# Optimization experiments

Measured on AMD Instinct MI355X. Metric: run time of the kernel, lower is better.

## Reference

```python
import jax, jax.numpy as jnp
from jax import lax
import numpy as np

B, T, IN = 32, 1024, 64
H1, H2, OUT = 512, 256, 1


def setup_inputs() -> dict:
    key = jax.random.key(0)
    ks = jax.random.split(key, 13)
    s = 0.05
    return {
        "x": jax.random.normal(ks[0], (B, T, IN), jnp.float32),
        # PyTorch LSTMCell params, gate order i,f,g,o stacked along first dim (4H)
        "W_ih0": jax.random.normal(ks[1], (4 * H1, IN), jnp.float32) * s,
        "W_hh0": jax.random.normal(ks[2], (4 * H1, H1), jnp.float32) * s,
        "b_ih0": jax.random.normal(ks[3], (4 * H1,), jnp.float32) * s,
        "b_hh0": jax.random.normal(ks[4], (4 * H1,), jnp.float32) * s,
        "W_ih1": jax.random.normal(ks[5], (4 * H1, H1), jnp.float32) * s,
        "W_hh1": jax.random.normal(ks[6], (4 * H1, H1), jnp.float32) * s,
        "b_ih1": jax.random.normal(ks[7], (4 * H1,), jnp.float32) * s,
        "b_hh1": jax.random.normal(ks[8], (4 * H1,), jnp.float32) * s,
        "W1": jax.random.normal(ks[9], (H2, H1), jnp.float32) * s,
        "b1": jax.random.normal(ks[10], (H2,), jnp.float32) * s,
        "W2": jax.random.normal(ks[11], (OUT, H2), jnp.float32) * s,
        "b2": jax.random.normal(ks[12], (OUT,), jnp.float32) * s,
    }


def _lstm_layer(x, W_ih, W_hh, b_ih, b_hh):
    """Unrolled LSTM layer. x: (B,T,F) -> hidden, cell sequences (B,T,H)."""
    b, t, _ = x.shape
    h = W_hh.shape[1]
    # precompute input contribution to gates for all timesteps: (B,T,4H)
    xg = jnp.einsum('btf,gf->btg', x, W_ih) + b_ih + b_hh

    def step(carry, xg_t):
        hx, cx = carry
        gates = xg_t + hx @ W_hh.T  # (B,4H)
        i, f, g, o = jnp.split(gates, 4, axis=-1)
        cx = jax.nn.sigmoid(f) * cx + jax.nn.sigmoid(i) * jnp.tanh(g)
        hx = jax.nn.sigmoid(o) * jnp.tanh(cx)
        return (hx, cx), (hx, cx)

    h0 = jnp.zeros((b, h), x.dtype)
    _, (hs, cs) = lax.scan(step, (h0, h0), jnp.swapaxes(xg, 0, 1))
    return jnp.swapaxes(hs, 0, 1), jnp.swapaxes(cs, 0, 1)


def reference(x, W_ih0, W_hh0, b_ih0, b_hh0, W_ih1, W_hh1, b_ih1, b_hh1,
              W1, b1, W2, b2):
    h0s, c0s = _lstm_layer(x, W_ih0, W_hh0, b_ih0, b_hh0)
    h1s, c1s = _lstm_layer(h0s, W_ih1, W_hh1, b_ih1, b_hh1)
    # MLP head (dropout layers are identity in eval mode)
    hidden = jax.nn.relu(h1s @ W1.T + b1)
    out = hidden @ W2.T + b2  # (B,T,OUT)
    return out, ((h0s, h1s), (c0s, c1s))
```

## Files before the change

kernel.cpp:

```cpp
#include <hip/hip_runtime.h>

#define HSEQ 16777216
#define NPL 32
#define NBLK 64

typedef __attribute__((ext_vector_type(8))) __bf16 bf16x8;
typedef __attribute__((ext_vector_type(4))) float f32x4;
typedef unsigned long long u64;

__global__ __launch_bounds__(256) void prep_x(const float* __restrict__ x,
                                              __bf16* __restrict__ xbf) {
    int idx = blockIdx.x * 256 + threadIdx.x;
    int k4 = idx & 15;
    int t  = (idx >> 4) & 1023;
    int m  = idx >> 14;
    float4 v = ((const float4*)x)[idx];
    __bf16* d = xbf + (size_t)t * 2048 + m * 64 + k4 * 4;
    d[0] = (__bf16)v.x; d[1] = (__bf16)v.y; d[2] = (__bf16)v.z; d[3] = (__bf16)v.w;
}

__device__ inline float sigf(float v) { return 1.f / (1.f + expf(-v)); }

__device__ __forceinline__ u64 llc_load(const u64* p) {
    return __hip_atomic_load(p, __ATOMIC_RELAXED, __HIP_MEMORY_SCOPE_AGENT);
}
__device__ __forceinline__ void llc_store(u64* p, u64 v) {
    __hip_atomic_store(p, v, __ATOMIC_RELAXED, __HIP_MEMORY_SCOPE_AGENT);
}

__device__ __forceinline__ void stfrag(char* smem, int kt_base, int m, int kc4, u64 v) {
    int k0   = kc4 << 2;
    int kt   = kt_base + (k0 >> 5);
    int sub  = (k0 >> 3) & 3;
    int half = (k0 >> 2) & 1;
    int slot = ((kt << 1) + (m >> 4)) * 64 + (sub << 4) + (m & 15);
    int byte = ((slot << 4) ^ (((slot >> 7) & 7) << 4)) + (half << 3);
    *(u64*)(smem + byte) = v;
}

template<int LAYER>
__device__ __forceinline__ void run_layer(
    int sub, int tid, int blk,
    const __bf16* __restrict__ xbf,
    const float* __restrict__ Wih, const float* __restrict__ Whh,
    const float* __restrict__ bih, const float* __restrict__ bhh,
    const __bf16* __restrict__ hin_buf,
    __bf16* __restrict__ hself_buf,
    int* flags,
    float* __restrict__ hs_out, float* __restrict__ cs_out,
    char* smem)
{
    constexpr int KT = LAYER ? 32 : 18;
    const int hd0   = sub * 16;
    const int lane  = tid & 63;
    const int wid   = tid >> 6;
    const int mtile = wid & 1;
    const int ntile = wid >> 1;
    const int koff  = (lane >> 4) << 3;

    bf16x8 wfr[KT];
    {
        const int n   = lane & 15;
        const int row = ntile * 512 + hd0 + n;
#pragma unroll
        for (int kt = 0; kt < KT; ++kt) {
            int k0 = kt * 32 + koff;
            const float* wp;
            if (LAYER == 0)
                wp = (k0 < 64) ? (Wih + (size_t)row * 64 + k0)
                               : (Whh + (size_t)row * 512 + (k0 - 64));
            else
                wp = (k0 < 512) ? (Wih + (size_t)row * 512 + k0)
                                : (Whh + (size_t)row * 512 + (k0 - 512));
            float4 f0 = ((const float4*)wp)[0];
            float4 f1 = ((const float4*)wp)[1];
            bf16x8 w;
            w[0]=(__bf16)f0.x; w[1]=(__bf16)f0.y; w[2]=(__bf16)f0.z; w[3]=(__bf16)f0.w;
            w[4]=(__bf16)f1.x; w[5]=(__bf16)f1.y; w[6]=(__bf16)f1.z; w[7]=(__bf16)f1.w;
            wfr[kt] = w;
        }
    }
    const int um = tid >> 4, uq = tid & 15;
    const float bi0 = bih[hd0 + uq]        + bhh[hd0 + uq];
    const float bi1 = bih[512 + hd0 + uq]  + bhh[512 + hd0 + uq];
    const float bi2 = bih[1024 + hd0 + uq] + bhh[1024 + hd0 + uq];
    const float bi3 = bih[1536 + hd0 + uq] + bhh[1536 + hd0 + uq];
    float creg = 0.f;

    float*  gates  = (float*)smem;
    __bf16* hstage = (__bf16*)(smem + 8448);

    for (int s = 0; s < 1025; ++s) {
        const bool active = LAYER ? (s >= 1) : (s < 1024);
        const int t = LAYER ? (s - 1) : s;

        if (s > 0 && tid < NBLK) {
            int* fp = flags + tid * 16;
            while (__hip_atomic_load(fp, __ATOMIC_RELAXED, __HIP_MEMORY_SCOPE_AGENT) < s)
                __builtin_amdgcn_s_sleep(1);
        }
        __syncthreads();

        if (active) {
            if (LAYER == 0) {
                u64 vx = *(const u64*)(xbf + (size_t)t * 2048 + (tid >> 4) * 64 + (tid & 15) * 4);
                const u64* hs = (const u64*)(hself_buf + ((s & 1) ^ 1) * (32 * 512));
                u64 v[8];
#pragma unroll
                for (int i = 0; i < 8; ++i) v[i] = llc_load(hs + tid + i * 512);
                stfrag(smem, 0, tid >> 4, tid & 15, vx);
#pragma unroll
                for (int i = 0; i < 8; ++i) {
                    int c = tid + i * 512;
                    stfrag(smem, 2, c >> 7, c & 127, v[i]);
                }
            } else {
                const u64* h0 = (const u64*)(hin_buf + ((s & 1) ^ 1) * (32 * 512));
                const u64* h1 = (const u64*)(hself_buf + ((s & 1) ^ 1) * (32 * 512));
                u64 v0[8], v1[8];
#pragma unroll
                for (int i = 0; i < 8; ++i) v0[i] = llc_load(h0 + tid + i * 512);
#pragma unroll
                for (int i = 0; i < 8; ++i) v1[i] = llc_load(h1 + tid + i * 512);
#pragma unroll
                for (int i = 0; i < 8; ++i) {
                    int c = tid + i * 512;
                    stfrag(smem, 0, c >> 7, c & 127, v0[i]);
                }
#pragma unroll
                for (int i = 0; i < 8; ++i) {
                    int c = tid + i * 512;
                    stfrag(smem, 16, c >> 7, c & 127, v1[i]);
                }
            }
        }
        __syncthreads();

        f32x4 acc0 = {0.f,0.f,0.f,0.f}, acc1 = {0.f,0.f,0.f,0.f};
        if (active) {
            const int sb = (mtile * 64 + lane) << 4;
#pragma unroll
            for (int kt = 0; kt < KT; ++kt) {
                bf16x8 a = *(const bf16x8*)(smem + ((sb ^ ((kt & 7) << 4)) + kt * 2048));
                if (kt & 1) acc1 = __builtin_amdgcn_mfma_f32_16x16x32_bf16(a, wfr[kt], acc1, 0, 0, 0);
                else        acc0 = __builtin_amdgcn_mfma_f32_16x16x32_bf16(a, wfr[kt], acc0, 0, 0, 0);
            }
        }
        __syncthreads();

        if (active) {
            f32x4 acc = acc0 + acc1;
#pragma unroll
            for (int r = 0; r < 4; ++r)
                gates[(mtile * 16 + ((lane >> 4) << 2) + r) * 65 + ntile * 16 + (lane & 15)] = acc[r];
        }
        __syncthreads();

        if (active) {
            float gi = gates[um * 65 + uq]      + bi0;
            float gf = gates[um * 65 + 16 + uq] + bi1;
            float gg = gates[um * 65 + 32 + uq] + bi2;
            float go = gates[um * 65 + 48 + uq] + bi3;
            float si = sigf(gi), sf = sigf(gf), so = sigf(go);
            creg = sf * creg + si * tanhf(gg);
            float hval = so * tanhf(creg);
            hstage[um * 16 + uq] = (__bf16)hval;
            __builtin_nontemporal_store(hval, &hs_out[((size_t)um * 1024 + t) * 512 + hd0 + uq]);
            __builtin_nontemporal_store(creg, &cs_out[((size_t)um * 1024 + t) * 512 + hd0 + uq]);
        }
        __syncthreads();

        if (active && tid < 128) {
            int m = tid >> 2, q4 = tid & 3;
            u64 v = *(const u64*)(hstage + m * 16 + q4 * 4);
            u64* hout = (u64*)(hself_buf + (s & 1) * (32 * 512));
            llc_store(hout + m * 128 + (hd0 >> 2) + q4, v);
        }
        __syncthreads();

        if (s < 1024 && tid == 0)
            __hip_atomic_store(flags + blk * 16, s + 1, __ATOMIC_RELAXED, __HIP_MEMORY_SCOPE_AGENT);
    }
}

__global__ __launch_bounds__(512, 1) void lstm2(
    const __bf16* __restrict__ xbf,
    const float* __restrict__ Wih0, const float* __restrict__ Whh0,
    const float* __restrict__ bih0, const float* __restrict__ bhh0,
    const float* __restrict__ Wih1, const float* __restrict__ Whh1,
    const float* __restrict__ bih1, const float* __restrict__ bhh1,
    __bf16* __restrict__ h0buf, __bf16* __restrict__ h1buf,
    int* flags, float* __restrict__ dout)
{
    __shared__ alignas(16) char smem[65536];
    const int tid = threadIdx.x, blk = blockIdx.x;
    float* hsbase = dout + 32768;
    if (blk < NPL)
        run_layer<0>(blk, tid, blk, xbf, Wih0, Whh0, bih0, bhh0, nullptr, h0buf,
                     flags, hsbase, hsbase + 2 * (size_t)HSEQ, smem);
    else
        run_layer<1>(blk - NPL, tid, blk, xbf, Wih1, Whh1, bih1, bhh1, h0buf, h1buf,
                     flags, hsbase + (size_t)HSEQ, hsbase + 3 * (size_t)HSEQ, smem);
}

__global__ __launch_bounds__(256) void head_kernel(
    const float* __restrict__ h1s, const float* __restrict__ W1,
    const float* __restrict__ b1,  const float* __restrict__ W2,
    const float* __restrict__ b2,  float* __restrict__ out)
{
    __shared__ alignas(16) float hl[16][512];
    __shared__ float red[16][257];
    const int tid = threadIdx.x;
    const size_t tok0 = (size_t)blockIdx.x * 16;

    const float4* src = (const float4*)(h1s + tok0 * 512);
    float4* dst = (float4*)(&hl[0][0]);
    for (int i = tid; i < 2048; i += 256) dst[i] = src[i];
    __syncthreads();

    float acc[16];
#pragma unroll
    for (int i = 0; i < 16; ++i) acc[i] = 0.f;
    const float4* wrow = (const float4*)(W1 + (size_t)tid * 512);
    for (int k4 = 0; k4 < 128; ++k4) {
        float4 w = wrow[k4];
#pragma unroll
        for (int i = 0; i < 16; ++i) {
            float4 h = ((const float4*)&hl[i][0])[k4];
            acc[i] += w.x * h.x + w.y * h.y + w.z * h.z + w.w * h.w;
        }
    }
    float w2 = W2[tid];
    float bb1 = b1[tid];
#pragma unroll
    for (int i = 0; i < 16; ++i) {
        float hid = acc[i] + bb1;
        red[i][tid] = w2 * (hid > 0.f ? hid : 0.f);
    }
    __syncthreads();
    if (tid < 16) {
        float ssum = b2[0];
        for (int j = 0; j < 256; ++j) ssum += red[tid][j];
        out[tok0 + tid] = ssum;
    }
}

extern "C" void kernel_launch(void* const* d_in, const int* in_sizes, int n_in,
                              void* d_out, int out_size, void* d_ws, size_t ws_size,
                              hipStream_t stream) {
    const float* x    = (const float*)d_in[0];
    const float* Wih0 = (const float*)d_in[1];
    const float* Whh0 = (const float*)d_in[2];
    const float* bih0 = (const float*)d_in[3];
    const float* bhh0 = (const float*)d_in[4];
    const float* Wih1 = (const float*)d_in[5];
    const float* Whh1 = (const float*)d_in[6];
    const float* bih1 = (const float*)d_in[7];
    const float* bhh1 = (const float*)d_in[8];
    const float* W1   = (const float*)d_in[9];
    const float* b1   = (const float*)d_in[10];
    const float* W2   = (const float*)d_in[11];
    const float* b2   = (const float*)d_in[12];
    float* out = (float*)d_out;

    char* ws = (char*)d_ws;
    int*    flags = (int*)ws;
    __bf16* h0buf = (__bf16*)(ws + 4096);
    __bf16* h1buf = (__bf16*)(ws + 4096 + 65536);
    __bf16* xbf   = (__bf16*)(ws + 4096 + 131072);

    hipMemsetAsync(ws, 0, 4096 + 131072, stream);

    prep_x<<<2048, 256, 0, stream>>>(x, xbf);

    const __bf16* xbf_c = xbf;
    void* args[] = {
        (void*)&xbf_c,
        (void*)&Wih0, (void*)&Whh0, (void*)&bih0, (void*)&bhh0,
        (void*)&Wih1, (void*)&Whh1, (void*)&bih1, (void*)&bhh1,
        (void*)&h0buf, (void*)&h1buf, (void*)&flags, (void*)&out
    };
    hipLaunchCooperativeKernel((const void*)lstm2, dim3(NBLK), dim3(512),
                               args, 0, stream);

    head_kernel<<<2048, 256, 0, stream>>>(out + 32768 + (size_t)HSEQ, W1, b1, W2, b2, out);
}
```

Measured before the change: 3.953 ms.

## Replace flag barrier with step-tagged hidden-state exchange and fewer block syncs

Each packed pair of bf16 hidden values is now stored together with its timestep in a 64-bit word. Consumers spin on these tags instead of polling per-block flag counters, so the global flag barrier and several __syncthreads per step go away. Layer 0 uses a 4-deep ring and a loose progress check against layer 1, which lets layer 0 run ahead of layer 1. The gate math switches to fast __expf-based sigmoid and tanh, with two units per thread and 64-bit output stores. The cost is doubled exchange traffic from the tag words, bounded spin loops that could silently give up, and slightly lower transcendental accuracy.

```diff
diff --git a/kernel.cpp b/kernel.cpp
--- a/kernel.cpp
+++ b/kernel.cpp
@@ -7,6 +7,7 @@
 typedef __attribute__((ext_vector_type(8))) __bf16 bf16x8;
 typedef __attribute__((ext_vector_type(4))) float f32x4;
 typedef unsigned long long u64;
+typedef unsigned int u32;
 
 __global__ __launch_bounds__(256) void prep_x(const float* __restrict__ x,
                                               __bf16* __restrict__ xbf) {
@@ -19,8 +20,6 @@
     d[0] = (__bf16)v.x; d[1] = (__bf16)v.y; d[2] = (__bf16)v.z; d[3] = (__bf16)v.w;
 }
 
-__device__ inline float sigf(float v) { return 1.f / (1.f + expf(-v)); }
-
 __device__ __forceinline__ u64 llc_load(const u64* p) {
     return __hip_atomic_load(p, __ATOMIC_RELAXED, __HIP_MEMORY_SCOPE_AGENT);
 }
@@ -28,27 +27,21 @@
     __hip_atomic_store(p, v, __ATOMIC_RELAXED, __HIP_MEMORY_SCOPE_AGENT);
 }
 
-__device__ __forceinline__ void stfrag(char* smem, int kt_base, int m, int kc4, u64 v) {
-    int k0   = kc4 << 2;
-    int kt   = kt_base + (k0 >> 5);
-    int sub  = (k0 >> 3) & 3;
-    int half = (k0 >> 2) & 1;
-    int slot = ((kt << 1) + (m >> 4)) * 64 + (sub << 4) + (m & 15);
-    int byte = ((slot << 4) ^ (((slot >> 7) & 7) << 4)) + (half << 3);
-    *(u64*)(smem + byte) = v;
+__device__ __forceinline__ float fsig(float v) { return 1.f / (1.f + __expf(-v)); }
+__device__ __forceinline__ float ftanh(float v) { return 1.f - 2.f / (__expf(2.f * v) + 1.f); }
+
+__device__ __forceinline__ int frag_byte(int kt, int mt, int sub, int r, int bis) {
+    return (((kt << 1) + mt) << 10) + (sub << 8) + (((r ^ sub ^ ((kt & 1) << 2)) & 15) << 4) + bis;
 }
 
 template<int LAYER>
-__device__ __forceinline__ void run_layer(
-    int sub, int tid, int blk,
+__device__ void run_layer(
+    int sub, int tid,
     const __bf16* __restrict__ xbf,
     const float* __restrict__ Wih, const float* __restrict__ Whh,
     const float* __restrict__ bih, const float* __restrict__ bhh,
-    const __bf16* __restrict__ hin_buf,
-    __bf16* __restrict__ hself_buf,
-    int* flags,
-    float* __restrict__ hs_out, float* __restrict__ cs_out,
-    char* smem)
+    u64* h0tag, u64* h1tag, u64* progress,
+    float* __restrict__ hs_out, float* __restrict__ cs_out, char* smem)
 {
     constexpr int KT = LAYER ? 32 : 18;
     const int hd0   = sub * 16;
@@ -80,127 +73,157 @@
             wfr[kt] = w;
         }
     }
-    const int um = tid >> 4, uq = tid & 15;
-    const float bi0 = bih[hd0 + uq]        + bhh[hd0 + uq];
-    const float bi1 = bih[512 + hd0 + uq]  + bhh[512 + hd0 + uq];
-    const float bi2 = bih[1024 + hd0 + uq] + bhh[1024 + hd0 + uq];
-    const float bi3 = bih[1536 + hd0 + uq] + bhh[1536 + hd0 + uq];
-    float creg = 0.f;
-
-    float*  gates  = (float*)smem;
-    __bf16* hstage = (__bf16*)(smem + 8448);
-
-    for (int s = 0; s < 1025; ++s) {
-        const bool active = LAYER ? (s >= 1) : (s < 1024);
-        const int t = LAYER ? (s - 1) : s;
-
-        if (s > 0 && tid < NBLK) {
-            int* fp = flags + tid * 16;
-            while (__hip_atomic_load(fp, __ATOMIC_RELAXED, __HIP_MEMORY_SCOPE_AGENT) < s)
-                __builtin_amdgcn_s_sleep(1);
+
+    const int um = tid >> 3, j2 = tid & 7;
+    float bg[4][2];
+    if (tid < 256) {
+#pragma unroll
+        for (int g = 0; g < 4; ++g)
+#pragma unroll
+            for (int p = 0; p < 2; ++p) {
+                int r = g * 512 + hd0 + 2 * j2 + p;
+                bg[g][p] = bih[r] + bhh[r];
+            }
+    }
+    float c0 = 0.f, c1 = 0.f;
+    float* gates = (float*)(smem + 65536);
+
+    const int rr = lane & 15, gg4 = lane >> 4;
+    const int S0 = LAYER ? 1 : 0;
+    const int S1 = LAYER ? 1025 : 1024;
+
+    for (int s = S0; s < S1; ++s) {
+        const int t = LAYER ? s - 1 : s;
+
+        if (LAYER == 0) {
+            if (s >= 3 && tid < NPL) {
+                u64* pp = progress + tid * 16;
+                int bound = 1 << 22;
+                while (llc_load(pp) < (u64)(s - 2) && --bound) __builtin_amdgcn_s_sleep(1);
+            }
+            int xm = tid >> 4, xc = tid & 15;
+            u64 vx = *(const u64*)(xbf + (size_t)t * 2048 + xm * 64 + xc * 4);
+
+            const u64* src = h0tag + (size_t)((s + 3) & 3) * 8192;
+            const u64 want = (u64)s;
+            u64 vals[16];
+            bool done = false;
+            int bound = 1 << 22;
+            while (!done && --bound) {
+                done = true;
+#pragma unroll
+                for (int i = 0; i < 16; ++i) vals[i] = llc_load(src + tid + i * 512);
+#pragma unroll
+                for (int i = 0; i < 16; ++i) done &= ((vals[i] >> 32) == want);
+            }
+            *(u64*)(smem + frag_byte(xc >> 3, xm >> 4, (xc >> 1) & 3, xm & 15, (xc & 1) << 3)) = vx;
+#pragma unroll
+            for (int i = 0; i < 16; ++i) {
+                int w = tid + i * 512;
+                int m = w >> 8, wq = w & 255;
+                *(u32*)(smem + frag_byte(2 + (wq >> 4), m >> 4, (wq >> 2) & 3, m & 15, (wq & 3) << 2))
+                    = (u32)vals[i];
+            }
+        } else {
+            const u64* srcA = h0tag + (size_t)((s + 3) & 3) * 8192;
+            const u64* srcB = h1tag + (size_t)((s + 1) & 1) * 8192;
+            const u64 wantA = (u64)s;
+            const u64 wantB = (s == 1) ? 0ull : (u64)s;
+            u64 va[16], vb[16];
+            bool done = false;
+            int bound = 1 << 22;
+            while (!done && --bound) {
+                done = true;
+#pragma unroll
+                for (int i = 0; i < 16; ++i) va[i] = llc_load(srcA + tid + i * 512);
+#pragma unroll
+                for (int i = 0; i < 16; ++i) vb[i] = llc_load(srcB + tid + i * 512);
+#pragma unroll
+                for (int i = 0; i < 16; ++i) done &= ((va[i] >> 32) == wantA);
+#pragma unroll
+                for (int i = 0; i < 16; ++i) done &= ((vb[i] >> 32) == wantB);
+            }
+#pragma unroll
+            for (int i = 0; i < 16; ++i) {
+                int w = tid + i * 512;
+                int m = w >> 8, wq = w & 255;
+                *(u32*)(smem + frag_byte(wq >> 4, m >> 4, (wq >> 2) & 3, m & 15, (wq & 3) << 2))
+                    = (u32)va[i];
+            }
+#pragma unroll
+            for (int i = 0; i < 16; ++i) {
+                int w = tid + i * 512;
+                int m = w >> 8, wq = w & 255;
+                *(u32*)(smem + frag_byte(16 + (wq >> 4), m >> 4, (wq >> 2) & 3, m & 15, (wq & 3) << 2))
+                    = (u32)vb[i];
+            }
         }
         __syncthreads();
 
-        if (active) {
-            if (LAYER == 0) {
-                u64 vx = *(const u64*)(xbf + (size_t)t * 2048 + (tid >> 4) * 64 + (tid & 15) * 4);
-                const u64* hs = (const u64*)(hself_buf + ((s & 1) ^ 1) * (32 * 512));
-                u64 v[8];
-#pragma unroll
-                for (int i = 0; i < 8; ++i) v[i] = llc_load(hs + tid + i * 512);
-                stfrag(smem, 0, tid >> 4, tid & 15, vx);
-#pragma unroll
-                for (int i = 0; i < 8; ++i) {
-                    int c = tid + i * 512;
-                    stfrag(smem, 2, c >> 7, c & 127, v[i]);
-                }
-            } else {
-                const u64* h0 = (const u64*)(hin_buf + ((s & 1) ^ 1) * (32 * 512));
-                const u64* h1 = (const u64*)(hself_buf + ((s & 1) ^ 1) * (32 * 512));
-                u64 v0[8], v1[8];
-#pragma unroll
-                for (int i = 0; i < 8; ++i) v0[i] = llc_load(h0 + tid + i * 512);
-#pragma unroll
-                for (int i = 0; i < 8; ++i) v1[i] = llc_load(h1 + tid + i * 512);
-#pragma unroll
-                for (int i = 0; i < 8; ++i) {
-                    int c = tid + i * 512;
-                    stfrag(smem, 0, c >> 7, c & 127, v0[i]);
-                }
-#pragma unroll
-                for (int i = 0; i < 8; ++i) {
-                    int c = tid + i * 512;
-                    stfrag(smem, 16, c >> 7, c & 127, v1[i]);
-                }
-            }
-        }
+        if (LAYER == 1 && tid == 0)
+            llc_store(progress + sub * 16, (u64)(s + 1));
+
+        f32x4 acc0 = {0.f,0.f,0.f,0.f}, acc1 = {0.f,0.f,0.f,0.f};
+#pragma unroll
+        for (int kt = 0; kt < KT; ++kt) {
+            bf16x8 a = *(const bf16x8*)(smem + frag_byte(kt, mtile, gg4, rr, 0));
+            if (kt & 1) acc1 = __builtin_amdgcn_mfma_f32_16x16x32_bf16(a, wfr[kt], acc1, 0, 0, 0);
+            else        acc0 = __builtin_amdgcn_mfma_f32_16x16x32_bf16(a, wfr[kt], acc0, 0, 0, 0);
+        }
+        f32x4 acc = acc0 + acc1;
+#pragma unroll
+        for (int r = 0; r < 4; ++r)
+            gates[(mtile * 16 + gg4 * 4 + r) * 65 + ntile * 16 + rr] = acc[r];
         __syncthreads();
 
-        f32x4 acc0 = {0.f,0.f,0.f,0.f}, acc1 = {0.f,0.f,0.f,0.f};
-        if (active) {
-            const int sb = (mtile * 64 + lane) << 4;
-#pragma unroll
-            for (int kt = 0; kt < KT; ++kt) {
-                bf16x8 a = *(const bf16x8*)(smem + ((sb ^ ((kt & 7) << 4)) + kt * 2048));
-                if (kt & 1) acc1 = __builtin_amdgcn_mfma_f32_16x16x32_bf16(a, wfr[kt], acc1, 0, 0, 0);
-                else        acc0 = __builtin_amdgcn_mfma_f32_16x16x32_bf16(a, wfr[kt], acc0, 0, 0, 0);
-            }
-        }
-        __syncthreads();
-
-        if (active) {
-            f32x4 acc = acc0 + acc1;
-#pragma unroll
-            for (int r = 0; r < 4; ++r)
-                gates[(mtile * 16 + ((lane >> 4) << 2) + r) * 65 + ntile * 16 + (lane & 15)] = acc[r];
-        }
-        __syncthreads();
-
-        if (active) {
-            float gi = gates[um * 65 + uq]      + bi0;
-            float gf = gates[um * 65 + 16 + uq] + bi1;
-            float gg = gates[um * 65 + 32 + uq] + bi2;
-            float go = gates[um * 65 + 48 + uq] + bi3;
-            float si = sigf(gi), sf = sigf(gf), so = sigf(go);
-            creg = sf * creg + si * tanhf(gg);
-            float hval = so * tanhf(creg);
-            hstage[um * 16 + uq] = (__bf16)hval;
-            __builtin_nontemporal_store(hval, &hs_out[((size_t)um * 1024 + t) * 512 + hd0 + uq]);
-            __builtin_nontemporal_store(creg, &cs_out[((size_t)um * 1024 + t) * 512 + hd0 + uq]);
-        }
-        __syncthreads();
-
-        if (active && tid < 128) {
-            int m = tid >> 2, q4 = tid & 3;
-            u64 v = *(const u64*)(hstage + m * 16 + q4 * 4);
-            u64* hout = (u64*)(hself_buf + (s & 1) * (32 * 512));
-            llc_store(hout + m * 128 + (hd0 >> 2) + q4, v);
-        }
-        __syncthreads();
-
-        if (s < 1024 && tid == 0)
-            __hip_atomic_store(flags + blk * 16, s + 1, __ATOMIC_RELAXED, __HIP_MEMORY_SCOPE_AGENT);
-    }
-}
-
-__global__ __launch_bounds__(512, 1) void lstm2(
+        if (tid < 256) {
+            const int q0 = 2 * j2;
+            float gi0 = gates[um * 65 + q0]          + bg[0][0];
+            float gi1 = gates[um * 65 + q0 + 1]      + bg[0][1];
+            float gf0 = gates[um * 65 + 16 + q0]     + bg[1][0];
+            float gf1 = gates[um * 65 + 16 + q0 + 1] + bg[1][1];
+            float gg0 = gates[um * 65 + 32 + q0]     + bg[2][0];
+            float gg1 = gates[um * 65 + 32 + q0 + 1] + bg[2][1];
+            float go0 = gates[um * 65 + 48 + q0]     + bg[3][0];
+            float go1 = gates[um * 65 + 48 + q0 + 1] + bg[3][1];
+            c0 = fsig(gf0) * c0 + fsig(gi0) * ftanh(gg0);
+            c1 = fsig(gf1) * c1 + fsig(gi1) * ftanh(gg1);
+            float h0v = fsig(go0) * ftanh(c0);
+            float h1v = fsig(go1) * ftanh(c1);
+
+            __bf16 hb0 = (__bf16)h0v, hb1 = (__bf16)h1v;
+            u32 pack = (u32)__builtin_bit_cast(unsigned short, hb0)
+                     | ((u32)__builtin_bit_cast(unsigned short, hb1) << 16);
+            u64* dst = LAYER ? (h1tag + (size_t)(s & 1) * 8192)
+                             : (h0tag + (size_t)(s & 3) * 8192);
+            llc_store(dst + um * 256 + sub * 8 + j2, ((u64)(s + 1) << 32) | (u64)pack);
+
+            size_t base = ((size_t)um * 1024 + t) * 512 + hd0 + q0;
+            u64 hv = (u64)__builtin_bit_cast(u32, h0v) | ((u64)__builtin_bit_cast(u32, h1v) << 32);
+            u64 cv = (u64)__builtin_bit_cast(u32, c0)  | ((u64)__builtin_bit_cast(u32, c1)  << 32);
+            __builtin_nontemporal_store(hv, (u64*)(hs_out + base));
+            __builtin_nontemporal_store(cv, (u64*)(cs_out + base));
+        }
+    }
+}
+
+__global__ __launch_bounds__(512, 2) void lstm2(
     const __bf16* __restrict__ xbf,
     const float* __restrict__ Wih0, const float* __restrict__ Whh0,
     const float* __restrict__ bih0, const float* __restrict__ bhh0,
     const float* __restrict__ Wih1, const float* __restrict__ Whh1,
     const float* __restrict__ bih1, const float* __restrict__ bhh1,
-    __bf16* __restrict__ h0buf, __bf16* __restrict__ h1buf,
-    int* flags, float* __restrict__ dout)
+    u64* h0tag, u64* h1tag, u64* progress, float* __restrict__ dout)
 {
-    __shared__ alignas(16) char smem[65536];
+    __shared__ alignas(16) char smem[73984];
     const int tid = threadIdx.x, blk = blockIdx.x;
     float* hsbase = dout + 32768;
     if (blk < NPL)
-        run_layer<0>(blk, tid, blk, xbf, Wih0, Whh0, bih0, bhh0, nullptr, h0buf,
-                     flags, hsbase, hsbase + 2 * (size_t)HSEQ, smem);
+        run_layer<0>(blk, tid, xbf, Wih0, Whh0, bih0, bhh0, h0tag, h1tag, progress,
+                     hsbase, hsbase + 2 * (size_t)HSEQ, smem);
     else
-        run_layer<1>(blk - NPL, tid, blk, xbf, Wih1, Whh1, bih1, bhh1, h0buf, h1buf,
-                     flags, hsbase + (size_t)HSEQ, hsbase + 3 * (size_t)HSEQ, smem);
+        run_layer<1>(blk - NPL, tid, xbf, Wih1, Whh1, bih1, bhh1, h0tag, h1tag, progress,
+                     hsbase + (size_t)HSEQ, hsbase + 3 * (size_t)HSEQ, smem);
 }
 
 __global__ __launch_bounds__(256) void head_kernel(
@@ -264,12 +287,12 @@
     float* out = (float*)d_out;
 
     char* ws = (char*)d_ws;
-    int*    flags = (int*)ws;
-    __bf16* h0buf = (__bf16*)(ws + 4096);
-    __bf16* h1buf = (__bf16*)(ws + 4096 + 65536);
-    __bf16* xbf   = (__bf16*)(ws + 4096 + 131072);
-
-    hipMemsetAsync(ws, 0, 4096 + 131072, stream);
+    u64* progress = (u64*)ws;
+    u64* h0tag    = (u64*)(ws + 4096);
+    u64* h1tag    = (u64*)(ws + 4096 + 262144);
+    __bf16* xbf   = (__bf16*)(ws + 4096 + 262144 + 131072);
+
+    hipMemsetAsync(ws, 0, 4096 + 262144 + 131072, stream);
 
     prep_x<<<2048, 256, 0, stream>>>(x, xbf);
 
@@ -278,7 +301,7 @@
         (void*)&xbf_c,
         (void*)&Wih0, (void*)&Whh0, (void*)&bih0, (void*)&bhh0,
         (void*)&Wih1, (void*)&Whh1, (void*)&bih1, (void*)&bhh1,
-        (void*)&h0buf, (void*)&h1buf, (void*)&flags, (void*)&out
+        (void*)&h0tag, (void*)&h1tag, (void*)&progress, (void*)&out
     };
     hipLaunchCooperativeKernel((const void*)lstm2, dim3(NBLK), dim3(512),
                                args, 0, stream);
```

Result: slower. 7.867 ms (+99.0%).
